# Kernel optimization log

Hardware: AMD Instinct MI355X
Metric: run time of the kernel (lower is better)

The kernel has to match this reference:

```python
import jax, jax.numpy as jnp
import numpy as np

B, T, I, H, O = 256, 100, 1024, 2048, 10

def setup_inputs() -> dict:
    key = jax.random.key(0)
    k = jax.random.split(key, 6)
    return {
        "x": jax.random.normal(k[0], (B, T, I), dtype=jnp.float32),
        "h0": jax.random.normal(k[1], (B, H), dtype=jnp.float32),
        "Win": jax.random.uniform(k[2], (I, H), dtype=jnp.float32, minval=-0.1, maxval=0.1),
        "W": jax.random.normal(k[3], (H, H), dtype=jnp.float32) * 0.01,
        "lin_w": jax.random.normal(k[4], (O, H), dtype=jnp.float32) * 0.02,
        "lin_b": jax.random.normal(k[5], (O,), dtype=jnp.float32) * 0.02,
    }

def reference(x, h0, Win, W, lin_w, lin_b):
    xin = jnp.einsum('bti,ih->bth', x, Win)  # precompute input projection for all steps

    def step(h, xin_t):
        h = jnp.tanh(xin_t + h @ W)
        y = h @ lin_w.T + lin_b
        return h, y

    _, ys = jax.lax.scan(step, h0, jnp.swapaxes(xin, 0, 1))  # ys: [T, B, O]
    return jnp.swapaxes(ys, 0, 1)  # [B, T, O]
```

## Files before the change

kernel.cpp:

```cpp
#include <hip/hip_runtime.h>
#include <math.h>

#define Bn 256
#define Tn 100
#define In 1024
#define Hn 2048
#define On 10
#define Kc (In + Hn)

typedef short s8v  __attribute__((ext_vector_type(8)));
typedef unsigned short us4 __attribute__((ext_vector_type(4)));
typedef float f32x4 __attribute__((ext_vector_type(4)));

__device__ __forceinline__ unsigned short f2bf(float f) {
    unsigned int u = __float_as_uint(f);
    u += 0x7fffu + ((u >> 16) & 1u);
    return (unsigned short)(u >> 16);
}

__device__ __forceinline__ float fast_tanh(float x) {
    float e = __expf(x + x);
    return 1.0f - 2.0f * __builtin_amdgcn_rcpf(e + 1.0f);
}


__global__ void conv_x_kernel(const float4* __restrict__ src, ushort4* __restrict__ dst) {
    int i = blockIdx.x * 256 + threadIdx.x;
    float4 v = src[i];
    ushort4 o;
    o.x = f2bf(v.x); o.y = f2bf(v.y); o.z = f2bf(v.z); o.w = f2bf(v.w);
    dst[i] = o;
}

__global__ void transpose_bf16_kernel(const float* __restrict__ src, unsigned short* __restrict__ dst,
                                      int N, int ld, int colOff) {
    __shared__ float tile[32][33];
    int k0 = blockIdx.x * 32;
    int n0 = blockIdx.y * 32;
    int c = threadIdx.x & 31;
    int r = threadIdx.x >> 5;
    #pragma unroll
    for (int i = 0; i < 32; i += 8)
        tile[r + i][c] = src[(size_t)(k0 + r + i) * N + n0 + c];
    __syncthreads();
    #pragma unroll
    for (int i = 0; i < 32; i += 8)
        dst[(size_t)(n0 + r + i) * ld + colOff + k0 + c] = f2bf(tile[c][r + i]);
}

__global__ void small_conv_kernel(const float* __restrict__ h0, const float* __restrict__ lin_w,
                                  unsigned short* __restrict__ h_all0, unsigned short* __restrict__ lwb,
                                  unsigned int* __restrict__ bar) {
    int idx = blockIdx.x * 256 + threadIdx.x;
    if (idx < 512) bar[idx] = 0u;
    if (idx < Bn * Hn) {
        h_all0[idx] = f2bf(h0[idx]);
    } else {
        int j = idx - Bn * Hn;
        int o = j >> 11;
        int k = j & 2047;
        lwb[j] = (o < On) ? f2bf(lin_w[o * Hn + k]) : (unsigned short)0;
    }
}

__global__ __launch_bounds__(512, 2)
void scan_kernel(const unsigned short* __restrict__ xb,
                 const unsigned short* __restrict__ BTm,
                 unsigned short* __restrict__ h_all,
                 unsigned int* __restrict__ bar) {
    const int g = blockIdx.x;
    const int mg = (g & 7) >> 1;
    const int m0 = mg * 64;
    const int nIdx = (g >> 3) * 2 + (g & 1);
    const int n0 = nIdx * 32;
    const int w = threadIdx.x >> 6;
    const int lane = threadIdx.x & 63;
    const int quad = lane >> 4;
    const int lr = lane & 15;
    const int hoff = nIdx & 7;
    const int xoff = nIdx & 3;

    __shared__ float red[8][64][36];

    const unsigned short* bp0 = BTm + (size_t)(n0 + lr) * Kc;
    const unsigned short* bp1 = BTm + (size_t)(n0 + 16 + lr) * Kc;

    const size_t xrow = (size_t)Tn * In;

    const int fidx = mg * 64 + (g & 1) * 32 + (g >> 3);
    unsigned int* fl = bar + mg * 64;

    s8v bx[4][2];
    s8v bh[8][2];
    #pragma unroll
    for (int c = 0; c < 4; ++c) {
        const int kq = w * 128 + (((c + xoff) & 3) * 32) + quad * 8;
        bx[c][0] = *(const s8v*)(bp0 + kq);
        bx[c][1] = *(const s8v*)(bp1 + kq);
    }
    #pragma unroll
    for (int c = 0; c < 8; ++c) {
        const int kq = In + w * 256 + (((c + hoff) & 7) * 32) + quad * 8;
        bh[c][0] = *(const s8v*)(bp0 + kq);
        bh[c][1] = *(const s8v*)(bp1 + kq);
    }

    f32x4 acc[4][2];
    #pragma unroll
    for (int mi = 0; mi < 4; ++mi)
        #pragma unroll
        for (int ni = 0; ni < 2; ++ni)
            acc[mi][ni] = (f32x4){0.f, 0.f, 0.f, 0.f};

    {
        const unsigned short* ar0 = xb + (size_t)(m0 + lr) * xrow + w * 128 + quad * 8;
        #pragma unroll
        for (int c = 0; c < 4; ++c) {
            const unsigned short* arow = ar0 + ((c + xoff) & 3) * 32;
            s8v a0 = *(const s8v*)(arow);
            s8v a1 = *(const s8v*)(arow + 16 * xrow);
            s8v a2 = *(const s8v*)(arow + 32 * xrow);
            s8v a3 = *(const s8v*)(arow + 48 * xrow);
            acc[0][0] = __builtin_amdgcn_mfma_f32_16x16x32_bf16(a0, bx[c][0], acc[0][0], 0, 0, 0);
            acc[1][0] = __builtin_amdgcn_mfma_f32_16x16x32_bf16(a1, bx[c][0], acc[1][0], 0, 0, 0);
            acc[2][0] = __builtin_amdgcn_mfma_f32_16x16x32_bf16(a2, bx[c][0], acc[2][0], 0, 0, 0);
            acc[3][0] = __builtin_amdgcn_mfma_f32_16x16x32_bf16(a3, bx[c][0], acc[3][0], 0, 0, 0);
            acc[0][1] = __builtin_amdgcn_mfma_f32_16x16x32_bf16(a0, bx[c][1], acc[0][1], 0, 0, 0);
            acc[1][1] = __builtin_amdgcn_mfma_f32_16x16x32_bf16(a1, bx[c][1], acc[1][1], 0, 0, 0);
            acc[2][1] = __builtin_amdgcn_mfma_f32_16x16x32_bf16(a2, bx[c][1], acc[2][1], 0, 0, 0);
            acc[3][1] = __builtin_amdgcn_mfma_f32_16x16x32_bf16(a3, bx[c][1], acc[3][1], 0, 0, 0);
        }
    }

    for (int t = 0; t < Tn; ++t) {
        const unsigned short* hrow = h_all + (size_t)t * (Bn * Hn)
                                   + (size_t)(m0 + lr) * Hn + w * 256 + quad * 8;
        s8v A[2][4];
        #pragma unroll
        for (int r = 0; r < 4; ++r)
            A[0][r] = *(const s8v*)(hrow + hoff * 32 + r * 16 * Hn);
        #pragma unroll
        for (int c = 0; c < 8; ++c) {
            if (c < 7) {
                const unsigned short* p = hrow + ((c + 1 + hoff) & 7) * 32;
                #pragma unroll
                for (int r = 0; r < 4; ++r)
                    A[(c + 1) & 1][r] = *(const s8v*)(p + r * 16 * Hn);
            }
            const s8v a0 = A[c & 1][0];
            const s8v a1 = A[c & 1][1];
            const s8v a2 = A[c & 1][2];
            const s8v a3 = A[c & 1][3];
            acc[0][0] = __builtin_amdgcn_mfma_f32_16x16x32_bf16(a0, bh[c][0], acc[0][0], 0, 0, 0);
            acc[1][0] = __builtin_amdgcn_mfma_f32_16x16x32_bf16(a1, bh[c][0], acc[1][0], 0, 0, 0);
            acc[2][0] = __builtin_amdgcn_mfma_f32_16x16x32_bf16(a2, bh[c][0], acc[2][0], 0, 0, 0);
            acc[3][0] = __builtin_amdgcn_mfma_f32_16x16x32_bf16(a3, bh[c][0], acc[3][0], 0, 0, 0);
            acc[0][1] = __builtin_amdgcn_mfma_f32_16x16x32_bf16(a0, bh[c][1], acc[0][1], 0, 0, 0);
            acc[1][1] = __builtin_amdgcn_mfma_f32_16x16x32_bf16(a1, bh[c][1], acc[1][1], 0, 0, 0);
            acc[2][1] = __builtin_amdgcn_mfma_f32_16x16x32_bf16(a2, bh[c][1], acc[2][1], 0, 0, 0);
            acc[3][1] = __builtin_amdgcn_mfma_f32_16x16x32_bf16(a3, bh[c][1], acc[3][1], 0, 0, 0);
        }

        #pragma unroll
        for (int mi = 0; mi < 4; ++mi)
            #pragma unroll
            for (int ni = 0; ni < 2; ++ni)
                #pragma unroll
                for (int rr = 0; rr < 4; ++rr)
                    red[w][mi * 16 + quad * 4 + rr][ni * 16 + lr] = acc[mi][ni][rr];

        s8v X[2][4];
        const unsigned short* arn = xb + (size_t)(t + 1) * In
                                  + (size_t)(m0 + lr) * xrow + w * 128 + quad * 8;
        if (t < Tn - 1) {
            #pragma unroll
            for (int c = 0; c < 2; ++c) {
                const unsigned short* p = arn + ((c + xoff) & 3) * 32;
                #pragma unroll
                for (int r = 0; r < 4; ++r)
                    X[c][r] = *(const s8v*)(p + r * 16 * xrow);
            }
        }

        __builtin_amdgcn_sched_barrier(0);
        asm volatile("s_waitcnt lgkmcnt(0)" ::: "memory");
        __builtin_amdgcn_s_barrier();
        __builtin_amdgcn_sched_barrier(0);

        {
            int j = threadIdx.x << 2;
            int row = j >> 5;
            int c0 = j & 31;
            float4 s0 = *(const float4*)&red[0][row][c0];
            float4 s1 = *(const float4*)&red[1][row][c0];
            float4 s2 = *(const float4*)&red[2][row][c0];
            float4 s3 = *(const float4*)&red[3][row][c0];
            float4 s4 = *(const float4*)&red[4][row][c0];
            float4 s5 = *(const float4*)&red[5][row][c0];
            float4 s6 = *(const float4*)&red[6][row][c0];
            float4 s7 = *(const float4*)&red[7][row][c0];
            us4 o4;
            o4[0] = f2bf(fast_tanh(((s0.x + s1.x) + (s2.x + s3.x)) + ((s4.x + s5.x) + (s6.x + s7.x))));
            o4[1] = f2bf(fast_tanh(((s0.y + s1.y) + (s2.y + s3.y)) + ((s4.y + s5.y) + (s6.y + s7.y))));
            o4[2] = f2bf(fast_tanh(((s0.z + s1.z) + (s2.z + s3.z)) + ((s4.z + s5.z) + (s6.z + s7.z))));
            o4[3] = f2bf(fast_tanh(((s0.w + s1.w) + (s2.w + s3.w)) + ((s4.w + s5.w) + (s6.w + s7.w))));
            unsigned long long* dst = (unsigned long long*)
                (h_all + (size_t)(t + 1) * (Bn * Hn) + (size_t)(m0 + row) * Hn + n0 + c0);
            __hip_atomic_store(dst, __builtin_bit_cast(unsigned long long, o4),
                               __ATOMIC_RELAXED, __HIP_MEMORY_SCOPE_AGENT);
        }

        if (t < Tn - 1) {
            __syncthreads();
            const unsigned int tp1 = (unsigned int)(t + 1);

            if (threadIdx.x == 0)
                __hip_atomic_store(bar + fidx, tp1, __ATOMIC_RELAXED,
                                   __HIP_MEMORY_SCOPE_AGENT);

            #pragma unroll
            for (int mi = 0; mi < 4; ++mi)
                #pragma unroll
                for (int ni = 0; ni < 2; ++ni)
                    acc[mi][ni] = (f32x4){0.f, 0.f, 0.f, 0.f};
            #pragma unroll
            for (int c = 0; c < 2; ++c) {
                acc[0][0] = __builtin_amdgcn_mfma_f32_16x16x32_bf16(X[c][0], bx[c][0], acc[0][0], 0, 0, 0);
                acc[1][0] = __builtin_amdgcn_mfma_f32_16x16x32_bf16(X[c][1], bx[c][0], acc[1][0], 0, 0, 0);
                acc[2][0] = __builtin_amdgcn_mfma_f32_16x16x32_bf16(X[c][2], bx[c][0], acc[2][0], 0, 0, 0);
                acc[3][0] = __builtin_amdgcn_mfma_f32_16x16x32_bf16(X[c][3], bx[c][0], acc[3][0], 0, 0, 0);
                acc[0][1] = __builtin_amdgcn_mfma_f32_16x16x32_bf16(X[c][0], bx[c][1], acc[0][1], 0, 0, 0);
                acc[1][1] = __builtin_amdgcn_mfma_f32_16x16x32_bf16(X[c][1], bx[c][1], acc[1][1], 0, 0, 0);
                acc[2][1] = __builtin_amdgcn_mfma_f32_16x16x32_bf16(X[c][2], bx[c][1], acc[2][1], 0, 0, 0);
                acc[3][1] = __builtin_amdgcn_mfma_f32_16x16x32_bf16(X[c][3], bx[c][1], acc[3][1], 0, 0, 0);
            }
            #pragma unroll
            for (int c = 2; c < 4; ++c) {
                const unsigned short* p = arn + ((c + xoff) & 3) * 32;
                s8v a0 = *(const s8v*)(p);
                s8v a1 = *(const s8v*)(p + 16 * xrow);
                s8v a2 = *(const s8v*)(p + 32 * xrow);
                s8v a3 = *(const s8v*)(p + 48 * xrow);
                acc[0][0] = __builtin_amdgcn_mfma_f32_16x16x32_bf16(a0, bx[c][0], acc[0][0], 0, 0, 0);
                acc[1][0] = __builtin_amdgcn_mfma_f32_16x16x32_bf16(a1, bx[c][0], acc[1][0], 0, 0, 0);
                acc[2][0] = __builtin_amdgcn_mfma_f32_16x16x32_bf16(a2, bx[c][0], acc[2][0], 0, 0, 0);
                acc[3][0] = __builtin_amdgcn_mfma_f32_16x16x32_bf16(a3, bx[c][0], acc[3][0], 0, 0, 0);
                acc[0][1] = __builtin_amdgcn_mfma_f32_16x16x32_bf16(a0, bx[c][1], acc[0][1], 0, 0, 0);
                acc[1][1] = __builtin_amdgcn_mfma_f32_16x16x32_bf16(a1, bx[c][1], acc[1][1], 0, 0, 0);
                acc[2][1] = __builtin_amdgcn_mfma_f32_16x16x32_bf16(a2, bx[c][1], acc[2][1], 0, 0, 0);
                acc[3][1] = __builtin_amdgcn_mfma_f32_16x16x32_bf16(a3, bx[c][1], acc[3][1], 0, 0, 0);
            }

            if (w == 0) {
                while (true) {
                    unsigned int v = __hip_atomic_load(fl + lane, __ATOMIC_RELAXED,
                                                       __HIP_MEMORY_SCOPE_AGENT);
                    if (__all((int)(v >= tp1))) break;
                    __builtin_amdgcn_s_sleep(1);
                }
            }
            asm volatile("" ::: "memory");
            __builtin_amdgcn_s_barrier();
            __builtin_amdgcn_sched_barrier(0);
        }
    }
}

__global__ __launch_bounds__(256)
void gemm2_kernel(const unsigned short* __restrict__ h_all, const unsigned short* __restrict__ lwb,
                  const float* __restrict__ lb, float* __restrict__ y) {
    int gw = blockIdx.x * 4 + (threadIdx.x >> 6);
    int lane = threadIdx.x & 63, quad = lane >> 4, lr = lane & 15;
    int m0 = gw * 16;
    int t = m0 >> 8;
    int b0 = m0 & 255;
    const unsigned short* ah = h_all + ((size_t)(t + 1) * Bn + b0 + lr) * Hn + quad * 8;
    const unsigned short* bh = lwb + (size_t)lr * Hn + quad * 8;
    f32x4 acc0 = {0.f, 0.f, 0.f, 0.f}, acc1 = {0.f, 0.f, 0.f, 0.f};
    #pragma unroll
    for (int k0 = 0; k0 < Hn; k0 += 64) {
        s8v a0 = *(const s8v*)(ah + k0);
        s8v b0 = *(const s8v*)(bh + k0);
        acc0 = __builtin_amdgcn_mfma_f32_16x16x32_bf16(a0, b0, acc0, 0, 0, 0);
        s8v a1 = *(const s8v*)(ah + k0 + 32);
        s8v b1 = *(const s8v*)(bh + k0 + 32);
        acc1 = __builtin_amdgcn_mfma_f32_16x16x32_bf16(a1, b1, acc1, 0, 0, 0);
    }
    acc0 = acc0 + acc1;
    if (lr < On) {
        float bias = lb[lr];
        #pragma unroll
        for (int rr = 0; rr < 4; ++rr) {
            int b = b0 + quad * 4 + rr;
            y[(size_t)b * (Tn * On) + t * On + lr] = acc0[rr] + bias;
        }
    }
}


extern "C" void kernel_launch(void* const* d_in, const int* in_sizes, int n_in,
                              void* d_out, int out_size, void* d_ws, size_t ws_size,
                              hipStream_t stream) {
    const float* x   = (const float*)d_in[0];
    const float* h0  = (const float*)d_in[1];
    const float* Win = (const float*)d_in[2];
    const float* W   = (const float*)d_in[3];
    const float* lw  = (const float*)d_in[4];
    const float* lb  = (const float*)d_in[5];
    float* y = (float*)d_out;

    unsigned short* ws    = (unsigned short*)d_ws;
    unsigned short* xb    = ws;
    unsigned short* BTm   = xb + (size_t)Bn * Tn * In;
    unsigned short* h_all = BTm + (size_t)Hn * Kc;
    unsigned short* lwb   = h_all + (size_t)(Tn + 1) * Bn * Hn;
    unsigned int*   bar   = (unsigned int*)(lwb + 32768);

    conv_x_kernel<<<25600, 256, 0, stream>>>((const float4*)x, (ushort4*)xb);
    transpose_bf16_kernel<<<dim3(32, 64), 256, 0, stream>>>(Win, BTm, Hn, Kc, 0);
    transpose_bf16_kernel<<<dim3(64, 64), 256, 0, stream>>>(W, BTm, Hn, Kc, In);
    small_conv_kernel<<<2176, 256, 0, stream>>>(h0, lw, h_all, lwb, bar);

    scan_kernel<<<256, 512, 0, stream>>>(xb, BTm, h_all, bar);

    gemm2_kernel<<<400, 256, 0, stream>>>(h_all, lwb, lb, y);
}
```

Measured before the change: 1.313 ms.

## Stop keeping input weights in registers and deepen h-load prefetch to four chunks

The input-projection weight fragments are no longer held in registers for the whole recurrence. Each step reloads them from global memory next to the x-tile loads, which frees registers. Those registers are spent on a deeper prefetch of the hidden-state A operands: four chunks are loaded up front and refilled after each MFMA group, replacing the previous double buffer. This trades extra per-step weight reloads, which should mostly hit in cache, for better latency hiding on the serial critical path.

```diff
diff --git a/kernel.cpp b/kernel.cpp
--- a/kernel.cpp
+++ b/kernel.cpp
@@ -90,14 +90,7 @@
     const int fidx = mg * 64 + (g & 1) * 32 + (g >> 3);
     unsigned int* fl = bar + mg * 64;
 
-    s8v bx[4][2];
     s8v bh[8][2];
-    #pragma unroll
-    for (int c = 0; c < 4; ++c) {
-        const int kq = w * 128 + (((c + xoff) & 3) * 32) + quad * 8;
-        bx[c][0] = *(const s8v*)(bp0 + kq);
-        bx[c][1] = *(const s8v*)(bp1 + kq);
-    }
     #pragma unroll
     for (int c = 0; c < 8; ++c) {
         const int kq = In + w * 256 + (((c + hoff) & 7) * 32) + quad * 8;
@@ -113,44 +106,48 @@
             acc[mi][ni] = (f32x4){0.f, 0.f, 0.f, 0.f};
 
     {
+        s8v bx0[4], bx1[4];
+        #pragma unroll
+        for (int c = 0; c < 4; ++c) {
+            const int kq = w * 128 + (((c + xoff) & 3) * 32) + quad * 8;
+            bx0[c] = *(const s8v*)(bp0 + kq);
+            bx1[c] = *(const s8v*)(bp1 + kq);
+        }
         const unsigned short* ar0 = xb + (size_t)(m0 + lr) * xrow + w * 128 + quad * 8;
+        s8v X[4][4];
+        #pragma unroll
+        for (int c = 0; c < 4; ++c)
+            #pragma unroll
+            for (int r = 0; r < 4; ++r)
+                X[c][r] = *(const s8v*)(ar0 + ((c + xoff) & 3) * 32 + r * 16 * xrow);
         #pragma unroll
         for (int c = 0; c < 4; ++c) {
-            const unsigned short* arow = ar0 + ((c + xoff) & 3) * 32;
-            s8v a0 = *(const s8v*)(arow);
-            s8v a1 = *(const s8v*)(arow + 16 * xrow);
-            s8v a2 = *(const s8v*)(arow + 32 * xrow);
-            s8v a3 = *(const s8v*)(arow + 48 * xrow);
-            acc[0][0] = __builtin_amdgcn_mfma_f32_16x16x32_bf16(a0, bx[c][0], acc[0][0], 0, 0, 0);
-            acc[1][0] = __builtin_amdgcn_mfma_f32_16x16x32_bf16(a1, bx[c][0], acc[1][0], 0, 0, 0);
-            acc[2][0] = __builtin_amdgcn_mfma_f32_16x16x32_bf16(a2, bx[c][0], acc[2][0], 0, 0, 0);
-            acc[3][0] = __builtin_amdgcn_mfma_f32_16x16x32_bf16(a3, bx[c][0], acc[3][0], 0, 0, 0);
-            acc[0][1] = __builtin_amdgcn_mfma_f32_16x16x32_bf16(a0, bx[c][1], acc[0][1], 0, 0, 0);
-            acc[1][1] = __builtin_amdgcn_mfma_f32_16x16x32_bf16(a1, bx[c][1], acc[1][1], 0, 0, 0);
-            acc[2][1] = __builtin_amdgcn_mfma_f32_16x16x32_bf16(a2, bx[c][1], acc[2][1], 0, 0, 0);
-            acc[3][1] = __builtin_amdgcn_mfma_f32_16x16x32_bf16(a3, bx[c][1], acc[3][1], 0, 0, 0);
+            acc[0][0] = __builtin_amdgcn_mfma_f32_16x16x32_bf16(X[c][0], bx0[c], acc[0][0], 0, 0, 0);
+            acc[1][0] = __builtin_amdgcn_mfma_f32_16x16x32_bf16(X[c][1], bx0[c], acc[1][0], 0, 0, 0);
+            acc[2][0] = __builtin_amdgcn_mfma_f32_16x16x32_bf16(X[c][2], bx0[c], acc[2][0], 0, 0, 0);
+            acc[3][0] = __builtin_amdgcn_mfma_f32_16x16x32_bf16(X[c][3], bx0[c], acc[3][0], 0, 0, 0);
+            acc[0][1] = __builtin_amdgcn_mfma_f32_16x16x32_bf16(X[c][0], bx1[c], acc[0][1], 0, 0, 0);
+            acc[1][1] = __builtin_amdgcn_mfma_f32_16x16x32_bf16(X[c][1], bx1[c], acc[1][1], 0, 0, 0);
+            acc[2][1] = __builtin_amdgcn_mfma_f32_16x16x32_bf16(X[c][2], bx1[c], acc[2][1], 0, 0, 0);
+            acc[3][1] = __builtin_amdgcn_mfma_f32_16x16x32_bf16(X[c][3], bx1[c], acc[3][1], 0, 0, 0);
         }
     }
 
     for (int t = 0; t < Tn; ++t) {
         const unsigned short* hrow = h_all + (size_t)t * (Bn * Hn)
                                    + (size_t)(m0 + lr) * Hn + w * 256 + quad * 8;
-        s8v A[2][4];
-        #pragma unroll
-        for (int r = 0; r < 4; ++r)
-            A[0][r] = *(const s8v*)(hrow + hoff * 32 + r * 16 * Hn);
+        s8v A[4][4];
+        #pragma unroll
+        for (int c = 0; c < 4; ++c)
+            #pragma unroll
+            for (int r = 0; r < 4; ++r)
+                A[c][r] = *(const s8v*)(hrow + ((c + hoff) & 7) * 32 + r * 16 * Hn);
         #pragma unroll
         for (int c = 0; c < 8; ++c) {
-            if (c < 7) {
-                const unsigned short* p = hrow + ((c + 1 + hoff) & 7) * 32;
-                #pragma unroll
-                for (int r = 0; r < 4; ++r)
-                    A[(c + 1) & 1][r] = *(const s8v*)(p + r * 16 * Hn);
-            }
-            const s8v a0 = A[c & 1][0];
-            const s8v a1 = A[c & 1][1];
-            const s8v a2 = A[c & 1][2];
-            const s8v a3 = A[c & 1][3];
+            const s8v a0 = A[c & 3][0];
+            const s8v a1 = A[c & 3][1];
+            const s8v a2 = A[c & 3][2];
+            const s8v a3 = A[c & 3][3];
             acc[0][0] = __builtin_amdgcn_mfma_f32_16x16x32_bf16(a0, bh[c][0], acc[0][0], 0, 0, 0);
             acc[1][0] = __builtin_amdgcn_mfma_f32_16x16x32_bf16(a1, bh[c][0], acc[1][0], 0, 0, 0);
             acc[2][0] = __builtin_amdgcn_mfma_f32_16x16x32_bf16(a2, bh[c][0], acc[2][0], 0, 0, 0);
@@ -159,6 +156,11 @@
             acc[1][1] = __builtin_amdgcn_mfma_f32_16x16x32_bf16(a1, bh[c][1], acc[1][1], 0, 0, 0);
             acc[2][1] = __builtin_amdgcn_mfma_f32_16x16x32_bf16(a2, bh[c][1], acc[2][1], 0, 0, 0);
             acc[3][1] = __builtin_amdgcn_mfma_f32_16x16x32_bf16(a3, bh[c][1], acc[3][1], 0, 0, 0);
+            if (c < 4) {
+                #pragma unroll
+                for (int r = 0; r < 4; ++r)
+                    A[c & 3][r] = *(const s8v*)(hrow + ((c + 4 + hoff) & 7) * 32 + r * 16 * Hn);
+            }
         }
 
         #pragma unroll
@@ -218,6 +220,21 @@
                 __hip_atomic_store(bar + fidx, tp1, __ATOMIC_RELAXED,
                                    __HIP_MEMORY_SCOPE_AGENT);
 
+            s8v bx0[4], bx1[4];
+            #pragma unroll
+            for (int c = 0; c < 4; ++c) {
+                const int kq = w * 128 + (((c + xoff) & 3) * 32) + quad * 8;
+                bx0[c] = *(const s8v*)(bp0 + kq);
+                bx1[c] = *(const s8v*)(bp1 + kq);
+            }
+            s8v X2[2][4];
+            #pragma unroll
+            for (int c = 0; c < 2; ++c) {
+                const unsigned short* p = arn + ((c + 2 + xoff) & 3) * 32;
+                #pragma unroll
+                for (int r = 0; r < 4; ++r)
+                    X2[c][r] = *(const s8v*)(p + r * 16 * xrow);
+            }
             #pragma unroll
             for (int mi = 0; mi < 4; ++mi)
                 #pragma unroll
@@ -225,30 +242,25 @@
                     acc[mi][ni] = (f32x4){0.f, 0.f, 0.f, 0.f};
             #pragma unroll
             for (int c = 0; c < 2; ++c) {
-                acc[0][0] = __builtin_amdgcn_mfma_f32_16x16x32_bf16(X[c][0], bx[c][0], acc[0][0], 0, 0, 0);
-                acc[1][0] = __builtin_amdgcn_mfma_f32_16x16x32_bf16(X[c][1], bx[c][0], acc[1][0], 0, 0, 0);
-                acc[2][0] = __builtin_amdgcn_mfma_f32_16x16x32_bf16(X[c][2], bx[c][0], acc[2][0], 0, 0, 0);
-                acc[3][0] = __builtin_amdgcn_mfma_f32_16x16x32_bf16(X[c][3], bx[c][0], acc[3][0], 0, 0, 0);
-                acc[0][1] = __builtin_amdgcn_mfma_f32_16x16x32_bf16(X[c][0], bx[c][1], acc[0][1], 0, 0, 0);
-                acc[1][1] = __builtin_amdgcn_mfma_f32_16x16x32_bf16(X[c][1], bx[c][1], acc[1][1], 0, 0, 0);
-                acc[2][1] = __builtin_amdgcn_mfma_f32_16x16x32_bf16(X[c][2], bx[c][1], acc[2][1], 0, 0, 0);
-                acc[3][1] = __builtin_amdgcn_mfma_f32_16x16x32_bf16(X[c][3], bx[c][1], acc[3][1], 0, 0, 0);
-            }
-            #pragma unroll
-            for (int c = 2; c < 4; ++c) {
-                const unsigned short* p = arn + ((c + xoff) & 3) * 32;
-                s8v a0 = *(const s8v*)(p);
-                s8v a1 = *(const s8v*)(p + 16 * xrow);
-                s8v a2 = *(const s8v*)(p + 32 * xrow);
-                s8v a3 = *(const s8v*)(p + 48 * xrow);
-                acc[0][0] = __builtin_amdgcn_mfma_f32_16x16x32_bf16(a0, bx[c][0], acc[0][0], 0, 0, 0);
-                acc[1][0] = __builtin_amdgcn_mfma_f32_16x16x32_bf16(a1, bx[c][0], acc[1][0], 0, 0, 0);
-                acc[2][0] = __builtin_amdgcn_mfma_f32_16x16x32_bf16(a2, bx[c][0], acc[2][0], 0, 0, 0);
-                acc[3][0] = __builtin_amdgcn_mfma_f32_16x16x32_bf16(a3, bx[c][0], acc[3][0], 0, 0, 0);
-                acc[0][1] = __builtin_amdgcn_mfma_f32_16x16x32_bf16(a0, bx[c][1], acc[0][1], 0, 0, 0);
-                acc[1][1] = __builtin_amdgcn_mfma_f32_16x16x32_bf16(a1, bx[c][1], acc[1][1], 0, 0, 0);
-                acc[2][1] = __builtin_amdgcn_mfma_f32_16x16x32_bf16(a2, bx[c][1], acc[2][1], 0, 0, 0);
-                acc[3][1] = __builtin_amdgcn_mfma_f32_16x16x32_bf16(a3, bx[c][1], acc[3][1], 0, 0, 0);
+                acc[0][0] = __builtin_amdgcn_mfma_f32_16x16x32_bf16(X[c][0], bx0[c], acc[0][0], 0, 0, 0);
+                acc[1][0] = __builtin_amdgcn_mfma_f32_16x16x32_bf16(X[c][1], bx0[c], acc[1][0], 0, 0, 0);
+                acc[2][0] = __builtin_amdgcn_mfma_f32_16x16x32_bf16(X[c][2], bx0[c], acc[2][0], 0, 0, 0);
+                acc[3][0] = __builtin_amdgcn_mfma_f32_16x16x32_bf16(X[c][3], bx0[c], acc[3][0], 0, 0, 0);
+                acc[0][1] = __builtin_amdgcn_mfma_f32_16x16x32_bf16(X[c][0], bx1[c], acc[0][1], 0, 0, 0);
+                acc[1][1] = __builtin_amdgcn_mfma_f32_16x16x32_bf16(X[c][1], bx1[c], acc[1][1], 0, 0, 0);
+                acc[2][1] = __builtin_amdgcn_mfma_f32_16x16x32_bf16(X[c][2], bx1[c], acc[2][1], 0, 0, 0);
+                acc[3][1] = __builtin_amdgcn_mfma_f32_16x16x32_bf16(X[c][3], bx1[c], acc[3][1], 0, 0, 0);
+            }
+            #pragma unroll
+            for (int c = 0; c < 2; ++c) {
+                acc[0][0] = __builtin_amdgcn_mfma_f32_16x16x32_bf16(X2[c][0], bx0[c + 2], acc[0][0], 0, 0, 0);
+                acc[1][0] = __builtin_amdgcn_mfma_f32_16x16x32_bf16(X2[c][1], bx0[c + 2], acc[1][0], 0, 0, 0);
+                acc[2][0] = __builtin_amdgcn_mfma_f32_16x16x32_bf16(X2[c][2], bx0[c + 2], acc[2][0], 0, 0, 0);
+                acc[3][0] = __builtin_amdgcn_mfma_f32_16x16x32_bf16(X2[c][3], bx0[c + 2], acc[3][0], 0, 0, 0);
+                acc[0][1] = __builtin_amdgcn_mfma_f32_16x16x32_bf16(X2[c][0], bx1[c + 2], acc[0][1], 0, 0, 0);
+                acc[1][1] = __builtin_amdgcn_mfma_f32_16x16x32_bf16(X2[c][1], bx1[c + 2], acc[1][1], 0, 0, 0);
+                acc[2][1] = __builtin_amdgcn_mfma_f32_16x16x32_bf16(X2[c][2], bx1[c + 2], acc[2][1], 0, 0, 0);
+                acc[3][1] = __builtin_amdgcn_mfma_f32_16x16x32_bf16(X2[c][3], bx1[c + 2], acc[3][1], 0, 0, 0);
             }
 
             if (w == 0) {
```

Measured after the change: 1.479 ms. +12.6%, slower.

## Split each block's batch tile into two half-tiles with independent sync groups

Applied to the files above, without the earlier changes.

Each block now handles two 32-row batch halves (A and B) instead of one 64-row tile. The halves are processed in turn, each with its own flag group, reduction buffer and wait. The intent is that while one half waits on its peers' flags, the other half's matmul and input projection can proceed, shrinking the serial critical path of the recurrence. The cost is more barriers and flag polls per step and smaller MFMA batches. The block-to-tile mapping and flag layout also change, so the synchronisation has to be correct.

```diff
diff --git a/kernel.cpp b/kernel.cpp
--- a/kernel.cpp
+++ b/kernel.cpp
@@ -63,15 +63,65 @@
     }
 }
 
+
+__device__ __forceinline__ void hpart(f32x4 (&acc)[2][2], const s8v (&bh)[8][2],
+                                      const unsigned short* hrow, int hoff) {
+    s8v A2[2][2];
+    #pragma unroll
+    for (int r = 0; r < 2; ++r)
+        A2[0][r] = *(const s8v*)(hrow + hoff * 32 + r * 16 * Hn);
+    #pragma unroll
+    for (int c = 0; c < 8; ++c) {
+        if (c < 7) {
+            const unsigned short* p = hrow + ((c + 1 + hoff) & 7) * 32;
+            #pragma unroll
+            for (int r = 0; r < 2; ++r)
+                A2[(c + 1) & 1][r] = *(const s8v*)(p + r * 16 * Hn);
+        }
+        const s8v a0 = A2[c & 1][0];
+        const s8v a1 = A2[c & 1][1];
+        acc[0][0] = __builtin_amdgcn_mfma_f32_16x16x32_bf16(a0, bh[c][0], acc[0][0], 0, 0, 0);
+        acc[1][0] = __builtin_amdgcn_mfma_f32_16x16x32_bf16(a1, bh[c][0], acc[1][0], 0, 0, 0);
+        acc[0][1] = __builtin_amdgcn_mfma_f32_16x16x32_bf16(a0, bh[c][1], acc[0][1], 0, 0, 0);
+        acc[1][1] = __builtin_amdgcn_mfma_f32_16x16x32_bf16(a1, bh[c][1], acc[1][1], 0, 0, 0);
+    }
+}
+
+__device__ __forceinline__ void xpart(f32x4 (&acc)[2][2], const s8v (&bx)[4][2],
+                                      const unsigned short* ar, int xoff, size_t xrow) {
+    s8v X[4][2];
+    #pragma unroll
+    for (int c = 0; c < 4; ++c)
+        #pragma unroll
+        for (int r = 0; r < 2; ++r)
+            X[c][r] = *(const s8v*)(ar + ((c + xoff) & 3) * 32 + r * 16 * xrow);
+    #pragma unroll
+    for (int c = 0; c < 4; ++c) {
+        acc[0][0] = __builtin_amdgcn_mfma_f32_16x16x32_bf16(X[c][0], bx[c][0], acc[0][0], 0, 0, 0);
+        acc[1][0] = __builtin_amdgcn_mfma_f32_16x16x32_bf16(X[c][1], bx[c][0], acc[1][0], 0, 0, 0);
+        acc[0][1] = __builtin_amdgcn_mfma_f32_16x16x32_bf16(X[c][0], bx[c][1], acc[0][1], 0, 0, 0);
+        acc[1][1] = __builtin_amdgcn_mfma_f32_16x16x32_bf16(X[c][1], bx[c][1], acc[1][1], 0, 0, 0);
+    }
+}
+
+__device__ __forceinline__ void zero_acc(f32x4 (&acc)[2][2]) {
+    #pragma unroll
+    for (int mi = 0; mi < 2; ++mi)
+        #pragma unroll
+        for (int ni = 0; ni < 2; ++ni)
+            acc[mi][ni] = (f32x4){0.f, 0.f, 0.f, 0.f};
+}
+
 __global__ __launch_bounds__(512, 2)
 void scan_kernel(const unsigned short* __restrict__ xb,
                  const unsigned short* __restrict__ BTm,
                  unsigned short* __restrict__ h_all,
                  unsigned int* __restrict__ bar) {
     const int g = blockIdx.x;
-    const int mg = (g & 7) >> 1;
-    const int m0 = mg * 64;
-    const int nIdx = (g >> 3) * 2 + (g & 1);
+    const int cA = g & 3;
+    const int m0A = cA * 32;
+    const int m0B = 128 + m0A;
+    const int nIdx = g >> 2;
     const int n0 = nIdx * 32;
     const int w = threadIdx.x >> 6;
     const int lane = threadIdx.x & 63;
@@ -80,15 +130,18 @@
     const int hoff = nIdx & 7;
     const int xoff = nIdx & 3;
 
-    __shared__ float red[8][64][36];
+    __shared__ float redA[8][32][36];
+    __shared__ float redB[8][32][36];
 
     const unsigned short* bp0 = BTm + (size_t)(n0 + lr) * Kc;
     const unsigned short* bp1 = BTm + (size_t)(n0 + 16 + lr) * Kc;
 
     const size_t xrow = (size_t)Tn * In;
 
-    const int fidx = mg * 64 + (g & 1) * 32 + (g >> 3);
-    unsigned int* fl = bar + mg * 64;
+    unsigned int* flA = bar + cA * 64;
+    unsigned int* flB = bar + (4 + cA) * 64;
+    const int fA = cA * 64 + nIdx;
+    const int fB = (4 + cA) * 64 + nIdx;
 
     s8v bx[4][2];
     s8v bh[8][2];
@@ -105,163 +158,121 @@
         bh[c][1] = *(const s8v*)(bp1 + kq);
     }
 
-    f32x4 acc[4][2];
-    #pragma unroll
-    for (int mi = 0; mi < 4; ++mi)
-        #pragma unroll
-        for (int ni = 0; ni < 2; ++ni)
-            acc[mi][ni] = (f32x4){0.f, 0.f, 0.f, 0.f};
-
-    {
-        const unsigned short* ar0 = xb + (size_t)(m0 + lr) * xrow + w * 128 + quad * 8;
-        #pragma unroll
-        for (int c = 0; c < 4; ++c) {
-            const unsigned short* arow = ar0 + ((c + xoff) & 3) * 32;
-            s8v a0 = *(const s8v*)(arow);
-            s8v a1 = *(const s8v*)(arow + 16 * xrow);
-            s8v a2 = *(const s8v*)(arow + 32 * xrow);
-            s8v a3 = *(const s8v*)(arow + 48 * xrow);
-            acc[0][0] = __builtin_amdgcn_mfma_f32_16x16x32_bf16(a0, bx[c][0], acc[0][0], 0, 0, 0);
-            acc[1][0] = __builtin_amdgcn_mfma_f32_16x16x32_bf16(a1, bx[c][0], acc[1][0], 0, 0, 0);
-            acc[2][0] = __builtin_amdgcn_mfma_f32_16x16x32_bf16(a2, bx[c][0], acc[2][0], 0, 0, 0);
-            acc[3][0] = __builtin_amdgcn_mfma_f32_16x16x32_bf16(a3, bx[c][0], acc[3][0], 0, 0, 0);
-            acc[0][1] = __builtin_amdgcn_mfma_f32_16x16x32_bf16(a0, bx[c][1], acc[0][1], 0, 0, 0);
-            acc[1][1] = __builtin_amdgcn_mfma_f32_16x16x32_bf16(a1, bx[c][1], acc[1][1], 0, 0, 0);
-            acc[2][1] = __builtin_amdgcn_mfma_f32_16x16x32_bf16(a2, bx[c][1], acc[2][1], 0, 0, 0);
-            acc[3][1] = __builtin_amdgcn_mfma_f32_16x16x32_bf16(a3, bx[c][1], acc[3][1], 0, 0, 0);
-        }
-    }
+    f32x4 accA[2][2], accB[2][2];
+    zero_acc(accA);
+    zero_acc(accB);
+
+    xpart(accA, bx, xb + (size_t)(m0A + lr) * xrow + w * 128 + quad * 8, xoff, xrow);
+    xpart(accB, bx, xb + (size_t)(m0B + lr) * xrow + w * 128 + quad * 8, xoff, xrow);
 
     for (int t = 0; t < Tn; ++t) {
-        const unsigned short* hrow = h_all + (size_t)t * (Bn * Hn)
-                                   + (size_t)(m0 + lr) * Hn + w * 256 + quad * 8;
-        s8v A[2][4];
-        #pragma unroll
-        for (int r = 0; r < 4; ++r)
-            A[0][r] = *(const s8v*)(hrow + hoff * 32 + r * 16 * Hn);
-        #pragma unroll
-        for (int c = 0; c < 8; ++c) {
-            if (c < 7) {
-                const unsigned short* p = hrow + ((c + 1 + hoff) & 7) * 32;
-                #pragma unroll
-                for (int r = 0; r < 4; ++r)
-                    A[(c + 1) & 1][r] = *(const s8v*)(p + r * 16 * Hn);
+        const size_t hbase = (size_t)t * (Bn * Hn);
+        const size_t obase = (size_t)(t + 1) * (Bn * Hn);
+
+        if (t > 0) {
+            unsigned int* pf = flA + w * 8 + (lane & 7);
+            while (true) {
+                unsigned int v = __hip_atomic_load(pf, __ATOMIC_RELAXED,
+                                                   __HIP_MEMORY_SCOPE_AGENT);
+                if (__all((int)(v >= (unsigned int)t))) break;
+                __builtin_amdgcn_s_sleep(1);
             }
-            const s8v a0 = A[c & 1][0];
-            const s8v a1 = A[c & 1][1];
-            const s8v a2 = A[c & 1][2];
-            const s8v a3 = A[c & 1][3];
-            acc[0][0] = __builtin_amdgcn_mfma_f32_16x16x32_bf16(a0, bh[c][0], acc[0][0], 0, 0, 0);
-            acc[1][0] = __builtin_amdgcn_mfma_f32_16x16x32_bf16(a1, bh[c][0], acc[1][0], 0, 0, 0);
-            acc[2][0] = __builtin_amdgcn_mfma_f32_16x16x32_bf16(a2, bh[c][0], acc[2][0], 0, 0, 0);
-            acc[3][0] = __builtin_amdgcn_mfma_f32_16x16x32_bf16(a3, bh[c][0], acc[3][0], 0, 0, 0);
-            acc[0][1] = __builtin_amdgcn_mfma_f32_16x16x32_bf16(a0, bh[c][1], acc[0][1], 0, 0, 0);
-            acc[1][1] = __builtin_amdgcn_mfma_f32_16x16x32_bf16(a1, bh[c][1], acc[1][1], 0, 0, 0);
-            acc[2][1] = __builtin_amdgcn_mfma_f32_16x16x32_bf16(a2, bh[c][1], acc[2][1], 0, 0, 0);
-            acc[3][1] = __builtin_amdgcn_mfma_f32_16x16x32_bf16(a3, bh[c][1], acc[3][1], 0, 0, 0);
-        }
-
-        #pragma unroll
-        for (int mi = 0; mi < 4; ++mi)
+            asm volatile("" ::: "memory");
+        }
+        hpart(accA, bh, h_all + hbase + (size_t)(m0A + lr) * Hn + w * 256 + quad * 8, hoff);
+
+        #pragma unroll
+        for (int mi = 0; mi < 2; ++mi)
             #pragma unroll
             for (int ni = 0; ni < 2; ++ni)
                 #pragma unroll
                 for (int rr = 0; rr < 4; ++rr)
-                    red[w][mi * 16 + quad * 4 + rr][ni * 16 + lr] = acc[mi][ni][rr];
-
-        s8v X[2][4];
-        const unsigned short* arn = xb + (size_t)(t + 1) * In
-                                  + (size_t)(m0 + lr) * xrow + w * 128 + quad * 8;
-        if (t < Tn - 1) {
-            #pragma unroll
-            for (int c = 0; c < 2; ++c) {
-                const unsigned short* p = arn + ((c + xoff) & 3) * 32;
-                #pragma unroll
-                for (int r = 0; r < 4; ++r)
-                    X[c][r] = *(const s8v*)(p + r * 16 * xrow);
-            }
-        }
-
+                    redA[w][mi * 16 + quad * 4 + rr][ni * 16 + lr] = accA[mi][ni][rr];
         __builtin_amdgcn_sched_barrier(0);
         asm volatile("s_waitcnt lgkmcnt(0)" ::: "memory");
         __builtin_amdgcn_s_barrier();
         __builtin_amdgcn_sched_barrier(0);
-
         {
-            int j = threadIdx.x << 2;
+            int j = threadIdx.x << 1;
             int row = j >> 5;
             int c0 = j & 31;
-            float4 s0 = *(const float4*)&red[0][row][c0];
-            float4 s1 = *(const float4*)&red[1][row][c0];
-            float4 s2 = *(const float4*)&red[2][row][c0];
-            float4 s3 = *(const float4*)&red[3][row][c0];
-            float4 s4 = *(const float4*)&red[4][row][c0];
-            float4 s5 = *(const float4*)&red[5][row][c0];
-            float4 s6 = *(const float4*)&red[6][row][c0];
-            float4 s7 = *(const float4*)&red[7][row][c0];
-            us4 o4;
-            o4[0] = f2bf(fast_tanh(((s0.x + s1.x) + (s2.x + s3.x)) + ((s4.x + s5.x) + (s6.x + s7.x))));
-            o4[1] = f2bf(fast_tanh(((s0.y + s1.y) + (s2.y + s3.y)) + ((s4.y + s5.y) + (s6.y + s7.y))));
-            o4[2] = f2bf(fast_tanh(((s0.z + s1.z) + (s2.z + s3.z)) + ((s4.z + s5.z) + (s6.z + s7.z))));
-            o4[3] = f2bf(fast_tanh(((s0.w + s1.w) + (s2.w + s3.w)) + ((s4.w + s5.w) + (s6.w + s7.w))));
-            unsigned long long* dst = (unsigned long long*)
-                (h_all + (size_t)(t + 1) * (Bn * Hn) + (size_t)(m0 + row) * Hn + n0 + c0);
-            __hip_atomic_store(dst, __builtin_bit_cast(unsigned long long, o4),
-                               __ATOMIC_RELAXED, __HIP_MEMORY_SCOPE_AGENT);
-        }
-
+            float2 s0 = *(const float2*)&redA[0][row][c0];
+            float2 s1 = *(const float2*)&redA[1][row][c0];
+            float2 s2 = *(const float2*)&redA[2][row][c0];
+            float2 s3 = *(const float2*)&redA[3][row][c0];
+            float2 s4 = *(const float2*)&redA[4][row][c0];
+            float2 s5 = *(const float2*)&redA[5][row][c0];
+            float2 s6 = *(const float2*)&redA[6][row][c0];
+            float2 s7 = *(const float2*)&redA[7][row][c0];
+            float sx = ((s0.x + s1.x) + (s2.x + s3.x)) + ((s4.x + s5.x) + (s6.x + s7.x));
+            float sy = ((s0.y + s1.y) + (s2.y + s3.y)) + ((s4.y + s5.y) + (s6.y + s7.y));
+            unsigned int o = (unsigned int)f2bf(fast_tanh(sx))
+                           | ((unsigned int)f2bf(fast_tanh(sy)) << 16);
+            unsigned int* dst = (unsigned int*)
+                (h_all + obase + (size_t)(m0A + row) * Hn + n0 + c0);
+            __hip_atomic_store(dst, o, __ATOMIC_RELAXED, __HIP_MEMORY_SCOPE_AGENT);
+        }
+        __syncthreads();
         if (t < Tn - 1) {
-            __syncthreads();
-            const unsigned int tp1 = (unsigned int)(t + 1);
-
             if (threadIdx.x == 0)
-                __hip_atomic_store(bar + fidx, tp1, __ATOMIC_RELAXED,
+                __hip_atomic_store(bar + fA, (unsigned int)(t + 1), __ATOMIC_RELAXED,
                                    __HIP_MEMORY_SCOPE_AGENT);
-
-            #pragma unroll
-            for (int mi = 0; mi < 4; ++mi)
-                #pragma unroll
-                for (int ni = 0; ni < 2; ++ni)
-                    acc[mi][ni] = (f32x4){0.f, 0.f, 0.f, 0.f};
-            #pragma unroll
-            for (int c = 0; c < 2; ++c) {
-                acc[0][0] = __builtin_amdgcn_mfma_f32_16x16x32_bf16(X[c][0], bx[c][0], acc[0][0], 0, 0, 0);
-                acc[1][0] = __builtin_amdgcn_mfma_f32_16x16x32_bf16(X[c][1], bx[c][0], acc[1][0], 0, 0, 0);
-                acc[2][0] = __builtin_amdgcn_mfma_f32_16x16x32_bf16(X[c][2], bx[c][0], acc[2][0], 0, 0, 0);
-                acc[3][0] = __builtin_amdgcn_mfma_f32_16x16x32_bf16(X[c][3], bx[c][0], acc[3][0], 0, 0, 0);
-                acc[0][1] = __builtin_amdgcn_mfma_f32_16x16x32_bf16(X[c][0], bx[c][1], acc[0][1], 0, 0, 0);
-                acc[1][1] = __builtin_amdgcn_mfma_f32_16x16x32_bf16(X[c][1], bx[c][1], acc[1][1], 0, 0, 0);
-                acc[2][1] = __builtin_amdgcn_mfma_f32_16x16x32_bf16(X[c][2], bx[c][1], acc[2][1], 0, 0, 0);
-                acc[3][1] = __builtin_amdgcn_mfma_f32_16x16x32_bf16(X[c][3], bx[c][1], acc[3][1], 0, 0, 0);
-            }
-            #pragma unroll
-            for (int c = 2; c < 4; ++c) {
-                const unsigned short* p = arn + ((c + xoff) & 3) * 32;
-                s8v a0 = *(const s8v*)(p);
-                s8v a1 = *(const s8v*)(p + 16 * xrow);
-                s8v a2 = *(const s8v*)(p + 32 * xrow);
-                s8v a3 = *(const s8v*)(p + 48 * xrow);
-                acc[0][0] = __builtin_amdgcn_mfma_f32_16x16x32_bf16(a0, bx[c][0], acc[0][0], 0, 0, 0);
-                acc[1][0] = __builtin_amdgcn_mfma_f32_16x16x32_bf16(a1, bx[c][0], acc[1][0], 0, 0, 0);
-                acc[2][0] = __builtin_amdgcn_mfma_f32_16x16x32_bf16(a2, bx[c][0], acc[2][0], 0, 0, 0);
-                acc[3][0] = __builtin_amdgcn_mfma_f32_16x16x32_bf16(a3, bx[c][0], acc[3][0], 0, 0, 0);
-                acc[0][1] = __builtin_amdgcn_mfma_f32_16x16x32_bf16(a0, bx[c][1], acc[0][1], 0, 0, 0);
-                acc[1][1] = __builtin_amdgcn_mfma_f32_16x16x32_bf16(a1, bx[c][1], acc[1][1], 0, 0, 0);
-                acc[2][1] = __builtin_amdgcn_mfma_f32_16x16x32_bf16(a2, bx[c][1], acc[2][1], 0, 0, 0);
-                acc[3][1] = __builtin_amdgcn_mfma_f32_16x16x32_bf16(a3, bx[c][1], acc[3][1], 0, 0, 0);
-            }
-
-            if (w == 0) {
-                while (true) {
-                    unsigned int v = __hip_atomic_load(fl + lane, __ATOMIC_RELAXED,
-                                                       __HIP_MEMORY_SCOPE_AGENT);
-                    if (__all((int)(v >= tp1))) break;
-                    __builtin_amdgcn_s_sleep(1);
-                }
+            zero_acc(accA);
+            xpart(accA, bx, xb + (size_t)(t + 1) * In + (size_t)(m0A + lr) * xrow
+                            + w * 128 + quad * 8, xoff, xrow);
+        }
+
+        if (t > 0) {
+            unsigned int* pf = flB + w * 8 + (lane & 7);
+            while (true) {
+                unsigned int v = __hip_atomic_load(pf, __ATOMIC_RELAXED,
+                                                   __HIP_MEMORY_SCOPE_AGENT);
+                if (__all((int)(v >= (unsigned int)t))) break;
+                __builtin_amdgcn_s_sleep(1);
             }
             asm volatile("" ::: "memory");
-            __builtin_amdgcn_s_barrier();
-            __builtin_amdgcn_sched_barrier(0);
+        }
+        hpart(accB, bh, h_all + hbase + (size_t)(m0B + lr) * Hn + w * 256 + quad * 8, hoff);
+
+        #pragma unroll
+        for (int mi = 0; mi < 2; ++mi)
+            #pragma unroll
+            for (int ni = 0; ni < 2; ++ni)
+                #pragma unroll
+                for (int rr = 0; rr < 4; ++rr)
+                    redB[w][mi * 16 + quad * 4 + rr][ni * 16 + lr] = accB[mi][ni][rr];
+        __builtin_amdgcn_sched_barrier(0);
+        asm volatile("s_waitcnt lgkmcnt(0)" ::: "memory");
+        __builtin_amdgcn_s_barrier();
+        __builtin_amdgcn_sched_barrier(0);
+        {
+            int j = threadIdx.x << 1;
+            int row = j >> 5;
+            int c0 = j & 31;
+            float2 s0 = *(const float2*)&redB[0][row][c0];
+            float2 s1 = *(const float2*)&redB[1][row][c0];
+            float2 s2 = *(const float2*)&redB[2][row][c0];
+            float2 s3 = *(const float2*)&redB[3][row][c0];
+            float2 s4 = *(const float2*)&redB[4][row][c0];
+            float2 s5 = *(const float2*)&redB[5][row][c0];
+            float2 s6 = *(const float2*)&redB[6][row][c0];
+            float2 s7 = *(const float2*)&redB[7][row][c0];
+            float sx = ((s0.x + s1.x) + (s2.x + s3.x)) + ((s4.x + s5.x) + (s6.x + s7.x));
+            float sy = ((s0.y + s1.y) + (s2.y + s3.y)) + ((s4.y + s5.y) + (s6.y + s7.y));
+            unsigned int o = (unsigned int)f2bf(fast_tanh(sx))
+                           | ((unsigned int)f2bf(fast_tanh(sy)) << 16);
+            unsigned int* dst = (unsigned int*)
+                (h_all + obase + (size_t)(m0B + row) * Hn + n0 + c0);
+            __hip_atomic_store(dst, o, __ATOMIC_RELAXED, __HIP_MEMORY_SCOPE_AGENT);
+        }
+        __syncthreads();
+        if (t < Tn - 1) {
+            if (threadIdx.x == 0)
+                __hip_atomic_store(bar + fB, (unsigned int)(t + 1), __ATOMIC_RELAXED,
+                                   __HIP_MEMORY_SCOPE_AGENT);
+            zero_acc(accB);
+            xpart(accB, bx, xb + (size_t)(t + 1) * In + (size_t)(m0B + lr) * xrow
+                            + w * 128 + quad * 8, xoff, xrow);
         }
     }
 }
```

After: 1.473 ms. 12.1% more time.
